# Kernel tuning notes

Hardware: AMD Instinct MI355X
Metric: run time of the kernel (lower is better)

## Reference

```python
import jax, jax.numpy as jnp
import numpy as np

BN_EPS = 1e-5

def binarize(v):
    # sign binarization with straight-through estimator (grad clipped to |v|<=1),
    # matching the Binarize autograd function used by BinarizeConv2d.
    c = jnp.clip(v, -1.0, 1.0)
    return c + jax.lax.stop_gradient(jnp.sign(v) - c)

def setup_inputs() -> dict:
    key = jax.random.key(0)
    kx, kw = jax.random.split(key)
    x = jax.random.normal(kx, (32, 64, 112, 112), dtype=jnp.float32)
    W = jax.random.normal(kw, (64, 64, 3, 3), dtype=jnp.float32) * 0.05
    gamma = jnp.ones((64,), dtype=jnp.float32)
    beta = jnp.zeros((64,), dtype=jnp.float32)
    return {"x": x, "W": W, "gamma": gamma, "beta": beta}

def reference(x, W, gamma, beta):
    residual = x
    # binet-style scaled binary conv: sign(x) * sign(W) conv, scaled per output
    # channel by alpha = mean(|W|) over (in, kh, kw)
    xb = binarize(x)
    wb = binarize(W)
    alpha = jnp.mean(jnp.abs(W), axis=(1, 2, 3))  # [Cout]
    out = jax.lax.conv_general_dilated(
        xb, wb,
        window_strides=(1, 1), padding=((1, 1), (1, 1)),
        dimension_numbers=("NCHW", "OIHW", "NCHW"))
    out = out * alpha[None, :, None, None]
    # BatchNorm2d (training mode: batch statistics over N,H,W)
    mu = jnp.mean(out, axis=(0, 2, 3), keepdims=True)
    var = jnp.var(out, axis=(0, 2, 3), keepdims=True)
    out = (out - mu) * jax.lax.rsqrt(var + BN_EPS)
    out = out * gamma[None, :, None, None] + beta[None, :, None, None]
    # Hardtanh
    out = jnp.clip(out, -1.0, 1.0)
    # residual add (downsample=None, stride=1)
    return out + residual
```

## Files before the change

### kernel.cpp

```cpp
#include <hip/hip_runtime.h>
#include <cstdint>

typedef unsigned long long u64;

#define HW    12544
#define NCH   64
#define NBATCH 32
#define NPIX  401408

__global__ __launch_bounds__(256) void k_pack(const float* __restrict__ x,
                                              const float* __restrict__ Wt,
                                              u64* __restrict__ xbits,
                                              u64* __restrict__ wbits,
                                              float* __restrict__ alpha) {
  int b = blockIdx.x;
  int t = threadIdx.x;
  if (b < 1568) {
    int n = b / 49;
    int p = (b % 49) * 256 + t;
    const float* xp = x + (size_t)n * NCH * HW + p;
    u64 m = 0;
#pragma unroll 16
    for (int c = 0; c < 64; ++c) {
      m |= (u64)(xp[(size_t)c * HW] > 0.0f) << c;
    }
    xbits[(size_t)n * HW + p] = m;
  } else {
    int wv = t >> 6, lane = t & 63;
    for (int i = 0; i < 16; ++i) {
      int co = wv * 16 + i;
      const float* wp = Wt + ((size_t)co * 64 + lane) * 9;
      float w9[9];
      float s = 0.0f;
#pragma unroll
      for (int k = 0; k < 9; ++k) { w9[k] = wp[k]; s += fabsf(w9[k]); }
#pragma unroll
      for (int off = 32; off > 0; off >>= 1) s += __shfl_xor(s, off);
#pragma unroll
      for (int k = 0; k < 9; ++k) {
        u64 msk = __ballot(w9[k] > 0.0f);
        if (lane == 0) wbits[k * 64 + co] = msk;
      }
      if (lane == 0) alpha[co] = s * (1.0f / 576.0f);
    }
  }
}

__global__ __launch_bounds__(256) void k_stats(const u64* __restrict__ xbits,
                                               const u64* __restrict__ wbits,
                                               u64* __restrict__ S1,
                                               u64* __restrict__ S2) {
  __shared__ u64 stg[4][114];
  __shared__ int corr[9][64];
  __shared__ int red1[256];
  __shared__ int red2[256];
  int b = blockIdx.x, t = threadIdx.x;
  int n = b / 56, h0 = (b % 56) * 2;

  for (int i = t; i < 4 * 114; i += 256) {
    int r = i / 114, cc = i % 114;
    int h = h0 - 1 + r, w = cc - 1;
    u64 v = 0;
    if (h >= 0 && h < 112 && (unsigned)w < 112u)
      v = xbits[(size_t)n * HW + h * 112 + w];
    stg[r][cc] = v;
  }

  int c = t & 63, wv = t >> 6;
  u64 wm[9];
#pragma unroll
  for (int k = 0; k < 9; ++k) wm[k] = wbits[k * 64 + c];

  if (t < 64) {
    int pw[9];
#pragma unroll
    for (int k = 0; k < 9; ++k) pw[k] = __popcll(wm[k]);
#pragma unroll
    for (int ht = 0; ht < 3; ++ht)
#pragma unroll
      for (int wt = 0; wt < 3; ++wt) {
        int s = 0;
#pragma unroll
        for (int k = 0; k < 9; ++k) {
          int dh = k / 3 - 1, dw = k % 3 - 1;
          bool inval = (ht == 0 && dh < 0) || (ht == 2 && dh > 0) ||
                       (wt == 0 && dw < 0) || (wt == 2 && dw > 0);
          if (inval) s += 64 - 2 * pw[k];
        }
        corr[ht * 3 + wt][t] = s;
      }
  }
  __syncthreads();

  int s1 = 0, s2 = 0;
  for (int k = 0; k < 56; ++k) {
    int pl = wv * 56 + k;
    int hl = pl / 112, w = pl % 112;
    int h = h0 + hl;
    int ht = (h == 0) ? 0 : ((h == 111) ? 2 : 1);
    int wt = (w == 0) ? 0 : ((w == 111) ? 2 : 1);
    int sum = 0;
#pragma unroll
    for (int kk = 0; kk < 9; ++kk)
      sum += __popcll(stg[hl + kk / 3][w + kk % 3] ^ wm[kk]);
    int I = 576 - 2 * sum - corr[ht * 3 + wt][c];
    s1 += I;
    s2 += I * I;
  }
  red1[t] = s1; red2[t] = s2;
  __syncthreads();
  if (t < 64) {
    int a1 = red1[t] + red1[t + 64] + red1[t + 128] + red1[t + 192];
    int a2 = red2[t] + red2[t + 64] + red2[t + 128] + red2[t + 192];
    atomicAdd(&S1[t], (u64)(long long)a1);
    atomicAdd(&S2[t], (u64)(long long)a2);
  }
}

__global__ __launch_bounds__(256) void k_final(const float* __restrict__ x,
                                               const u64* __restrict__ xbits,
                                               const u64* __restrict__ wbits,
                                               const u64* __restrict__ S1,
                                               const u64* __restrict__ S2,
                                               const float* __restrict__ alpha,
                                               const float* __restrict__ gamma,
                                               const float* __restrict__ beta,
                                               float* __restrict__ out) {
  __shared__ u64 stg[4][114];
  __shared__ u64 wsh[576];
  __shared__ int corr[9][64];
  __shared__ float scs[64];
  __shared__ float bis[64];
  int b = blockIdx.x, t = threadIdx.x;
  int n = b / 56, h0 = (b % 56) * 2;

  for (int i = t; i < 4 * 114; i += 256) {
    int r = i / 114, cc = i % 114;
    int h = h0 - 1 + r, w = cc - 1;
    u64 v = 0;
    if (h >= 0 && h < 112 && (unsigned)w < 112u)
      v = xbits[(size_t)n * HW + h * 112 + w];
    stg[r][cc] = v;
  }
  for (int i = t; i < 576; i += 256) wsh[i] = wbits[i];

  if (t < 64) {
    int pw[9];
#pragma unroll
    for (int k = 0; k < 9; ++k) pw[k] = __popcll(wbits[k * 64 + t]);
#pragma unroll
    for (int ht = 0; ht < 3; ++ht)
#pragma unroll
      for (int wt = 0; wt < 3; ++wt) {
        int s = 0;
#pragma unroll
        for (int k = 0; k < 9; ++k) {
          int dh = k / 3 - 1, dw = k % 3 - 1;
          bool inval = (ht == 0 && dh < 0) || (ht == 2 && dh > 0) ||
                       (wt == 0 && dw < 0) || (wt == 2 && dw > 0);
          if (inval) s += 64 - 2 * pw[k];
        }
        corr[ht * 3 + wt][t] = s;
      }
    long long s1 = (long long)S1[t];
    long long s2 = (long long)S2[t];
    double inv = 1.0 / (double)NPIX;
    double mean = (double)s1 * inv;
    double var = (double)s2 * inv - mean * mean;
    double al = (double)alpha[t];
    double rs = 1.0 / sqrt(al * al * var + 1e-5);
    double sc = (double)gamma[t] * al * rs;
    scs[t] = (float)sc;
    bis[t] = (float)((double)beta[t] - sc * mean);
  }
  __syncthreads();

  if (t < 224) {
    int hl = t / 112, w = t % 112;
    int h = h0 + hl;
    int ht = (h == 0) ? 0 : ((h == 111) ? 2 : 1);
    int wt = (w == 0) ? 0 : ((w == 111) ? 2 : 1);
    int type = ht * 3 + wt;
    u64 xm[9];
#pragma unroll
    for (int kk = 0; kk < 9; ++kk) xm[kk] = stg[hl + kk / 3][w + kk % 3];
    const float* xp = x + (size_t)n * NCH * HW + (size_t)h * 112 + w;
    float* op = out + (size_t)n * NCH * HW + (size_t)h * 112 + w;
#pragma unroll 4
    for (int c = 0; c < 64; ++c) {
      int sum = 0;
#pragma unroll
      for (int kk = 0; kk < 9; ++kk) sum += __popcll(xm[kk] ^ wsh[kk * 64 + c]);
      int I = 576 - 2 * sum - corr[type][c];
      float o = fmaf((float)I, scs[c], bis[c]);
      o = fminf(fmaxf(o, -1.0f), 1.0f);
      op[(size_t)c * HW] = o + xp[(size_t)c * HW];
    }
  }
}

extern "C" void kernel_launch(void* const* d_in, const int* in_sizes, int n_in,
                              void* d_out, int out_size, void* d_ws, size_t ws_size,
                              hipStream_t stream) {
  const float* x     = (const float*)d_in[0];
  const float* W     = (const float*)d_in[1];
  const float* gamma = (const float*)d_in[2];
  const float* beta  = (const float*)d_in[3];
  float* out = (float*)d_out;

  char* ws = (char*)d_ws;
  u64*  S1    = (u64*)(ws + 0);
  u64*  S2    = (u64*)(ws + 512);
  float* alpha = (float*)(ws + 1024);
  u64*  wbits = (u64*)(ws + 2048);
  u64*  xbits = (u64*)(ws + 8192);

  hipMemsetAsync(ws, 0, 1024, stream);

  hipLaunchKernelGGL(k_pack, dim3(1569), dim3(256), 0, stream, x, W, xbits, wbits, alpha);
  hipLaunchKernelGGL(k_stats, dim3(32 * 56), dim3(256), 0, stream, xbits, wbits, S1, S2);
  hipLaunchKernelGGL(k_final, dim3(32 * 56), dim3(256), 0, stream,
                     x, xbits, wbits, S1, S2, alpha, gamma, beta, out);
}
```

Baseline: 276.6 us.

## Register-block 4 rows per thread in binary conv kernels and vectorize packing

After: 266.8 us. 1.04x faster.

```diff
diff --git a/kernel.cpp b/kernel.cpp
--- a/kernel.cpp
+++ b/kernel.cpp
@@ -4,28 +4,34 @@
 typedef unsigned long long u64;
 
 #define HW    12544
-#define NCH   64
-#define NBATCH 32
 #define NPIX  401408
 
 __global__ __launch_bounds__(256) void k_pack(const float* __restrict__ x,
                                               const float* __restrict__ Wt,
                                               u64* __restrict__ xbits,
                                               u64* __restrict__ wbits,
-                                              float* __restrict__ alpha) {
+                                              float* __restrict__ alpha,
+                                              u64* __restrict__ stats) {
   int b = blockIdx.x;
   int t = threadIdx.x;
-  if (b < 1568) {
-    int n = b / 49;
-    int p = (b % 49) * 256 + t;
-    const float* xp = x + (size_t)n * NCH * HW + p;
-    u64 m = 0;
-#pragma unroll 16
+  if (b < 392) {
+    int gp = (b * 256 + t) * 4;
+    int n = gp / HW, p = gp % HW;
+    const float* xp = x + (size_t)n * 64 * HW + p;
+    u64 m0 = 0, m1 = 0, m2 = 0, m3 = 0;
+#pragma unroll 8
     for (int c = 0; c < 64; ++c) {
-      m |= (u64)(xp[(size_t)c * HW] > 0.0f) << c;
+      const float4 v = *reinterpret_cast<const float4*>(xp + (size_t)c * HW);
+      m0 |= (u64)(v.x > 0.0f) << c;
+      m1 |= (u64)(v.y > 0.0f) << c;
+      m2 |= (u64)(v.z > 0.0f) << c;
+      m3 |= (u64)(v.w > 0.0f) << c;
     }
-    xbits[(size_t)n * HW + p] = m;
+    ulonglong2* d2 = reinterpret_cast<ulonglong2*>(xbits + (size_t)n * HW + p);
+    d2[0] = make_ulonglong2(m0, m1);
+    d2[1] = make_ulonglong2(m2, m3);
   } else {
+    if (t < 128) stats[t] = 0;
     int wv = t >> 6, lane = t & 63;
     for (int i = 0; i < 16; ++i) {
       int co = wv * 16 + i;
@@ -50,70 +56,70 @@
                                                const u64* __restrict__ wbits,
                                                u64* __restrict__ S1,
                                                u64* __restrict__ S2) {
-  __shared__ u64 stg[4][114];
-  __shared__ int corr[9][64];
+  __shared__ u64 stg[10][114];
   __shared__ int red1[256];
   __shared__ int red2[256];
   int b = blockIdx.x, t = threadIdx.x;
-  int n = b / 56, h0 = (b % 56) * 2;
-
-  for (int i = t; i < 4 * 114; i += 256) {
+  int n = b / 14, h0 = (b % 14) * 8;
+
+  for (int i = t; i < 10 * 114; i += 256) {
     int r = i / 114, cc = i % 114;
     int h = h0 - 1 + r, w = cc - 1;
     u64 v = 0;
-    if (h >= 0 && h < 112 && (unsigned)w < 112u)
+    if ((unsigned)h < 112u && (unsigned)w < 112u)
       v = xbits[(size_t)n * HW + h * 112 + w];
     stg[r][cc] = v;
   }
 
   int c = t & 63, wv = t >> 6;
-  u64 wm[9];
-#pragma unroll
-  for (int k = 0; k < 9; ++k) wm[k] = wbits[k * 64 + c];
-
-  if (t < 64) {
-    int pw[9];
-#pragma unroll
-    for (int k = 0; k < 9; ++k) pw[k] = __popcll(wm[k]);
-#pragma unroll
-    for (int ht = 0; ht < 3; ++ht)
-#pragma unroll
-      for (int wt = 0; wt < 3; ++wt) {
-        int s = 0;
-#pragma unroll
-        for (int k = 0; k < 9; ++k) {
-          int dh = k / 3 - 1, dw = k % 3 - 1;
-          bool inval = (ht == 0 && dh < 0) || (ht == 2 && dh > 0) ||
-                       (wt == 0 && dw < 0) || (wt == 2 && dw > 0);
-          if (inval) s += 64 - 2 * pw[k];
-        }
-        corr[ht * 3 + wt][t] = s;
-      }
-  }
+  u64 wm0, wm1, wm2, wm3, wm4, wm5, wm6, wm7, wm8;
+  wm0 = wbits[0 * 64 + c]; wm1 = wbits[1 * 64 + c]; wm2 = wbits[2 * 64 + c];
+  wm3 = wbits[3 * 64 + c]; wm4 = wbits[4 * 64 + c]; wm5 = wbits[5 * 64 + c];
+  wm6 = wbits[6 * 64 + c]; wm7 = wbits[7 * 64 + c]; wm8 = wbits[8 * 64 + c];
+  int pw0 = __popcll(wm0), pw1 = __popcll(wm1), pw2 = __popcll(wm2);
+  int pw3 = __popcll(wm3), pw4 = __popcll(wm4), pw5 = __popcll(wm5);
+  int pw6 = __popcll(wm6), pw7 = __popcll(wm7), pw8 = __popcll(wm8);
+  int vtop = (64-2*pw0) + (64-2*pw1) + (64-2*pw2);
+  int vbot = (64-2*pw6) + (64-2*pw7) + (64-2*pw8);
+  int hlft = (64-2*pw0) + (64-2*pw3) + (64-2*pw6);
+  int hrgt = (64-2*pw2) + (64-2*pw5) + (64-2*pw8);
+  int cTL = 64-2*pw0, cTR = 64-2*pw2, cBL = 64-2*pw6, cBR = 64-2*pw8;
   __syncthreads();
 
   int s1 = 0, s2 = 0;
-  for (int k = 0; k < 56; ++k) {
-    int pl = wv * 56 + k;
-    int hl = pl / 112, w = pl % 112;
-    int h = h0 + hl;
-    int ht = (h == 0) ? 0 : ((h == 111) ? 2 : 1);
-    int wt = (w == 0) ? 0 : ((w == 111) ? 2 : 1);
-    int sum = 0;
-#pragma unroll
-    for (int kk = 0; kk < 9; ++kk)
-      sum += __popcll(stg[hl + kk / 3][w + kk % 3] ^ wm[kk]);
-    int I = 576 - 2 * sum - corr[ht * 3 + wt][c];
-    s1 += I;
-    s2 += I * I;
+  for (int it = 0; it < 56; ++it) {
+    int idx = wv * 56 + it;
+    int s = idx / 112, w = idx % 112;
+    int r0 = s * 4;
+    u64 a0 = stg[r0+0][w], a1 = stg[r0+0][w+1], a2 = stg[r0+0][w+2];
+    u64 b0 = stg[r0+1][w], b1 = stg[r0+1][w+1], b2 = stg[r0+1][w+2];
+    u64 c0 = stg[r0+2][w], c1 = stg[r0+2][w+1], c2 = stg[r0+2][w+2];
+    u64 d0 = stg[r0+3][w], d1 = stg[r0+3][w+1], d2 = stg[r0+3][w+2];
+    u64 e0 = stg[r0+4][w], e1 = stg[r0+4][w+1], e2 = stg[r0+4][w+2];
+    u64 f0 = stg[r0+5][w], f1 = stg[r0+5][w+1], f2 = stg[r0+5][w+2];
+    int wl = (w == 0), wr = (w == 111);
+    int hcor = wl ? hlft : (wr ? hrgt : 0);
+    int ctop = hcor, cbot = hcor;
+    if (h0 + s * 4 == 0)        ctop += vtop - (wl ? cTL : 0) - (wr ? cTR : 0);
+    if (h0 + s * 4 + 3 == 111)  cbot += vbot - (wl ? cBL : 0) - (wr ? cBR : 0);
+#define PX(x0,x1,x2,x3,x4,x5,x6,x7,x8,corr)                                    \
+    { int sum = __popcll((x0)^wm0)+__popcll((x1)^wm1)+__popcll((x2)^wm2)       \
+              + __popcll((x3)^wm3)+__popcll((x4)^wm4)+__popcll((x5)^wm5)       \
+              + __popcll((x6)^wm6)+__popcll((x7)^wm7)+__popcll((x8)^wm8);      \
+      int I = 576 - 2*sum - (corr); s1 += I; s2 += I*I; }
+    PX(a0,a1,a2,b0,b1,b2,c0,c1,c2, ctop);
+    PX(b0,b1,b2,c0,c1,c2,d0,d1,d2, hcor);
+    PX(c0,c1,c2,d0,d1,d2,e0,e1,e2, hcor);
+    PX(d0,d1,d2,e0,e1,e2,f0,f1,f2, cbot);
+#undef PX
   }
   red1[t] = s1; red2[t] = s2;
   __syncthreads();
   if (t < 64) {
-    int a1 = red1[t] + red1[t + 64] + red1[t + 128] + red1[t + 192];
-    int a2 = red2[t] + red2[t + 64] + red2[t + 128] + red2[t + 192];
-    atomicAdd(&S1[t], (u64)(long long)a1);
-    atomicAdd(&S2[t], (u64)(long long)a2);
+    int a1s = red1[t] + red1[t+64] + red1[t+128] + red1[t+192];
+    int a2s = red2[t] + red2[t+64] + red2[t+128] + red2[t+192];
+    atomicAdd(&S1[t], (u64)(long long)a1s);
+    atomicAdd(&S2[t], (u64)(long long)a2s);
   }
 }
 
@@ -126,19 +132,19 @@
                                                const float* __restrict__ gamma,
                                                const float* __restrict__ beta,
                                                float* __restrict__ out) {
-  __shared__ u64 stg[4][114];
+  __shared__ u64 stg[10][114];
   __shared__ u64 wsh[576];
-  __shared__ int corr[9][64];
+  __shared__ int corrs[9 * 64];
   __shared__ float scs[64];
   __shared__ float bis[64];
   int b = blockIdx.x, t = threadIdx.x;
-  int n = b / 56, h0 = (b % 56) * 2;
-
-  for (int i = t; i < 4 * 114; i += 256) {
+  int n = b / 14, h0 = (b % 14) * 8;
+
+  for (int i = t; i < 10 * 114; i += 256) {
     int r = i / 114, cc = i % 114;
     int h = h0 - 1 + r, w = cc - 1;
     u64 v = 0;
-    if (h >= 0 && h < 112 && (unsigned)w < 112u)
+    if ((unsigned)h < 112u && (unsigned)w < 112u)
       v = xbits[(size_t)n * HW + h * 112 + w];
     stg[r][cc] = v;
   }
@@ -160,7 +166,7 @@
                        (wt == 0 && dw < 0) || (wt == 2 && dw > 0);
           if (inval) s += 64 - 2 * pw[k];
         }
-        corr[ht * 3 + wt][t] = s;
+        corrs[(ht * 3 + wt) * 64 + t] = s;
       }
     long long s1 = (long long)S1[t];
     long long s2 = (long long)S2[t];
@@ -176,25 +182,50 @@
   __syncthreads();
 
   if (t < 224) {
-    int hl = t / 112, w = t % 112;
-    int h = h0 + hl;
-    int ht = (h == 0) ? 0 : ((h == 111) ? 2 : 1);
-    int wt = (w == 0) ? 0 : ((w == 111) ? 2 : 1);
-    int type = ht * 3 + wt;
-    u64 xm[9];
-#pragma unroll
-    for (int kk = 0; kk < 9; ++kk) xm[kk] = stg[hl + kk / 3][w + kk % 3];
-    const float* xp = x + (size_t)n * NCH * HW + (size_t)h * 112 + w;
-    float* op = out + (size_t)n * NCH * HW + (size_t)h * 112 + w;
-#pragma unroll 4
+    int w = t % 112, s = t / 112;
+    int r0 = s * 4;
+    int hb = h0 + s * 4;
+    u64 a0 = stg[r0+0][w], a1 = stg[r0+0][w+1], a2 = stg[r0+0][w+2];
+    u64 b0 = stg[r0+1][w], b1 = stg[r0+1][w+1], b2 = stg[r0+1][w+2];
+    u64 c0 = stg[r0+2][w], c1 = stg[r0+2][w+1], c2 = stg[r0+2][w+2];
+    u64 d0 = stg[r0+3][w], d1 = stg[r0+3][w+1], d2 = stg[r0+3][w+2];
+    u64 e0 = stg[r0+4][w], e1 = stg[r0+4][w+1], e2 = stg[r0+4][w+2];
+    u64 f0 = stg[r0+5][w], f1 = stg[r0+5][w+1], f2 = stg[r0+5][w+2];
+    int wl = (w == 0), wr = (w == 111);
+    int wt = wl ? 0 : (wr ? 2 : 1);
+    int ttop = ((hb == 0) ? 0 : 1) * 3 + wt;
+    int tmid = 3 + wt;
+    int tbot = ((hb + 3 == 111) ? 2 : 1) * 3 + wt;
+    const float* xp = x + (size_t)n * 64 * HW + (size_t)hb * 112 + w;
+    float* op = out + (size_t)n * 64 * HW + (size_t)hb * 112 + w;
+#pragma unroll 2
     for (int c = 0; c < 64; ++c) {
-      int sum = 0;
-#pragma unroll
-      for (int kk = 0; kk < 9; ++kk) sum += __popcll(xm[kk] ^ wsh[kk * 64 + c]);
-      int I = 576 - 2 * sum - corr[type][c];
-      float o = fmaf((float)I, scs[c], bis[c]);
-      o = fminf(fmaxf(o, -1.0f), 1.0f);
-      op[(size_t)c * HW] = o + xp[(size_t)c * HW];
+      int off = c * HW;
+      float x0 = xp[off], x1 = xp[off + 112], x2 = xp[off + 224], x3 = xp[off + 336];
+      u64 w0 = wsh[c],       w1 = wsh[64 + c],  w2 = wsh[128 + c];
+      u64 w3 = wsh[192 + c], w4 = wsh[256 + c], w5 = wsh[320 + c];
+      u64 w6 = wsh[384 + c], w7 = wsh[448 + c], w8 = wsh[512 + c];
+      float sc = scs[c], bi = bis[c];
+      int ct = corrs[ttop * 64 + c];
+      int cm = corrs[tmid * 64 + c];
+      int cb = corrs[tbot * 64 + c];
+#define SUM9(x0_,x1_,x2_,x3_,x4_,x5_,x6_,x7_,x8_)                              \
+      (__popcll((x0_)^w0)+__popcll((x1_)^w1)+__popcll((x2_)^w2)                \
+      +__popcll((x3_)^w3)+__popcll((x4_)^w4)+__popcll((x5_)^w5)                \
+      +__popcll((x6_)^w6)+__popcll((x7_)^w7)+__popcll((x8_)^w8))
+      int I0 = 576 - 2 * SUM9(a0,a1,a2,b0,b1,b2,c0,c1,c2) - ct;
+      int I1 = 576 - 2 * SUM9(b0,b1,b2,c0,c1,c2,d0,d1,d2) - cm;
+      int I2 = 576 - 2 * SUM9(c0,c1,c2,d0,d1,d2,e0,e1,e2) - cm;
+      int I3 = 576 - 2 * SUM9(d0,d1,d2,e0,e1,e2,f0,f1,f2) - cb;
+#undef SUM9
+      float o0 = fminf(fmaxf(fmaf((float)I0, sc, bi), -1.0f), 1.0f);
+      float o1 = fminf(fmaxf(fmaf((float)I1, sc, bi), -1.0f), 1.0f);
+      float o2 = fminf(fmaxf(fmaf((float)I2, sc, bi), -1.0f), 1.0f);
+      float o3 = fminf(fmaxf(fmaf((float)I3, sc, bi), -1.0f), 1.0f);
+      op[off]       = o0 + x0;
+      op[off + 112] = o1 + x1;
+      op[off + 224] = o2 + x2;
+      op[off + 336] = o3 + x3;
     }
   }
 }
@@ -209,16 +240,16 @@
   float* out = (float*)d_out;
 
   char* ws = (char*)d_ws;
-  u64*  S1    = (u64*)(ws + 0);
-  u64*  S2    = (u64*)(ws + 512);
+  u64*   S1    = (u64*)(ws + 0);
+  u64*   S2    = (u64*)(ws + 512);
   float* alpha = (float*)(ws + 1024);
-  u64*  wbits = (u64*)(ws + 2048);
-  u64*  xbits = (u64*)(ws + 8192);
-
-  hipMemsetAsync(ws, 0, 1024, stream);
-
-  hipLaunchKernelGGL(k_pack, dim3(1569), dim3(256), 0, stream, x, W, xbits, wbits, alpha);
-  hipLaunchKernelGGL(k_stats, dim3(32 * 56), dim3(256), 0, stream, xbits, wbits, S1, S2);
-  hipLaunchKernelGGL(k_final, dim3(32 * 56), dim3(256), 0, stream,
+  u64*   wbits = (u64*)(ws + 2048);
+  u64*   xbits = (u64*)(ws + 8192);
+
+  hipLaunchKernelGGL(k_pack, dim3(393), dim3(256), 0, stream,
+                     x, W, xbits, wbits, alpha, (u64*)ws);
+  hipLaunchKernelGGL(k_stats, dim3(32 * 14), dim3(256), 0, stream,
+                     xbits, wbits, S1, S2);
+  hipLaunchKernelGGL(k_final, dim3(32 * 14), dim3(256), 0, stream,
                      x, xbits, wbits, S1, S2, alpha, gamma, beta, out);
 }
```

## Replace popcount binary conv with int8 MFMA on zero-padded ±1 activations

Applied to the files above, without the earlier changes.

Measured after the change: 369.1 us. 33.4% more time.

```diff
diff --git a/kernel.cpp b/kernel.cpp
--- a/kernel.cpp
+++ b/kernel.cpp
@@ -2,200 +2,204 @@
 #include <cstdint>
 
 typedef unsigned long long u64;
-
-#define HW    12544
-#define NCH   64
-#define NBATCH 32
-#define NPIX  401408
+typedef unsigned int u32;
+typedef int v4i __attribute__((ext_vector_type(4)));
+
+#define HW   12544
+#define NPIX 401408
+#define PROW 114
+#define PRB  (PROW * 64)
+#define PNB  (114 * PRB)
 
 __global__ __launch_bounds__(256) void k_pack(const float* __restrict__ x,
-                                              const float* __restrict__ Wt,
-                                              u64* __restrict__ xbits,
-                                              u64* __restrict__ wbits,
-                                              float* __restrict__ alpha) {
-  int b = blockIdx.x;
-  int t = threadIdx.x;
-  if (b < 1568) {
-    int n = b / 49;
-    int p = (b % 49) * 256 + t;
-    const float* xp = x + (size_t)n * NCH * HW + p;
-    u64 m = 0;
-#pragma unroll 16
+                                              const float* __restrict__ W,
+                                              unsigned char* __restrict__ xi8,
+                                              unsigned char* __restrict__ wi8,
+                                              float* __restrict__ alpha9,
+                                              u64* __restrict__ stats) {
+  int b = blockIdx.x, t = threadIdx.x;
+  if (b < 392) {
+    int gp = (b * 256 + t) * 4;
+    int n = gp / HW, p = gp % HW;
+    int h = p / 112, w = p % 112;
+    const float* xp = x + (size_t)(n * 64) * HW + p;
+    u32 wd[4][16];
+#pragma unroll
+    for (int px = 0; px < 4; ++px)
+#pragma unroll
+      for (int q = 0; q < 16; ++q) wd[px][q] = 0;
+#pragma unroll
     for (int c = 0; c < 64; ++c) {
-      m |= (u64)(xp[(size_t)c * HW] > 0.0f) << c;
-    }
-    xbits[(size_t)n * HW + p] = m;
+      float4 v = *reinterpret_cast<const float4*>(xp + (size_t)c * HW);
+      u32 sh = (u32)(c & 3) * 8; int q = c >> 2;
+      wd[0][q] |= (v.x > 0.f ? 0x01u : 0xFFu) << sh;
+      wd[1][q] |= (v.y > 0.f ? 0x01u : 0xFFu) << sh;
+      wd[2][q] |= (v.z > 0.f ? 0x01u : 0xFFu) << sh;
+      wd[3][q] |= (v.w > 0.f ? 0x01u : 0xFFu) << sh;
+    }
+    uint4* sp = reinterpret_cast<uint4*>(
+        xi8 + (size_t)n * PNB + (size_t)(h + 1) * PRB + (size_t)(w + 1) * 64);
+#pragma unroll
+    for (int px = 0; px < 4; ++px)
+#pragma unroll
+      for (int q4 = 0; q4 < 4; ++q4)
+        sp[px * 4 + q4] = make_uint4(wd[px][4*q4], wd[px][4*q4+1],
+                                     wd[px][4*q4+2], wd[px][4*q4+3]);
   } else {
-    int wv = t >> 6, lane = t & 63;
-    for (int i = 0; i < 16; ++i) {
-      int co = wv * 16 + i;
-      const float* wp = Wt + ((size_t)co * 64 + lane) * 9;
-      float w9[9];
-      float s = 0.0f;
-#pragma unroll
-      for (int k = 0; k < 9; ++k) { w9[k] = wp[k]; s += fabsf(w9[k]); }
-#pragma unroll
-      for (int off = 32; off > 0; off >>= 1) s += __shfl_xor(s, off);
-#pragma unroll
-      for (int k = 0; k < 9; ++k) {
-        u64 msk = __ballot(w9[k] > 0.0f);
-        if (lane == 0) wbits[k * 64 + co] = msk;
+    if (t < 128) stats[t] = 0;
+    for (int i = t; i < 576; i += 256) {
+      int tap = i / 64, co = i % 64;
+      u32 wdw[16];
+#pragma unroll
+      for (int q = 0; q < 16; ++q) wdw[q] = 0;
+      float asum = 0.f;
+#pragma unroll
+      for (int ci = 0; ci < 64; ++ci) {
+        float wv = W[((size_t)co * 64 + ci) * 9 + tap];
+        asum += fabsf(wv);
+        wdw[ci >> 2] |= (wv > 0.f ? 0x01u : 0xFFu) << ((u32)(ci & 3) * 8);
       }
-      if (lane == 0) alpha[co] = s * (1.0f / 576.0f);
-    }
-  }
-}
-
-__global__ __launch_bounds__(256) void k_stats(const u64* __restrict__ xbits,
-                                               const u64* __restrict__ wbits,
-                                               u64* __restrict__ S1,
-                                               u64* __restrict__ S2) {
-  __shared__ u64 stg[4][114];
-  __shared__ int corr[9][64];
-  __shared__ int red1[256];
-  __shared__ int red2[256];
-  int b = blockIdx.x, t = threadIdx.x;
-  int n = b / 56, h0 = (b % 56) * 2;
-
-  for (int i = t; i < 4 * 114; i += 256) {
-    int r = i / 114, cc = i % 114;
-    int h = h0 - 1 + r, w = cc - 1;
-    u64 v = 0;
-    if (h >= 0 && h < 112 && (unsigned)w < 112u)
-      v = xbits[(size_t)n * HW + h * 112 + w];
-    stg[r][cc] = v;
-  }
-
-  int c = t & 63, wv = t >> 6;
-  u64 wm[9];
-#pragma unroll
-  for (int k = 0; k < 9; ++k) wm[k] = wbits[k * 64 + c];
-
-  if (t < 64) {
-    int pw[9];
-#pragma unroll
-    for (int k = 0; k < 9; ++k) pw[k] = __popcll(wm[k]);
-#pragma unroll
-    for (int ht = 0; ht < 3; ++ht)
-#pragma unroll
-      for (int wt = 0; wt < 3; ++wt) {
-        int s = 0;
-#pragma unroll
-        for (int k = 0; k < 9; ++k) {
-          int dh = k / 3 - 1, dw = k % 3 - 1;
-          bool inval = (ht == 0 && dh < 0) || (ht == 2 && dh > 0) ||
-                       (wt == 0 && dw < 0) || (wt == 2 && dw > 0);
-          if (inval) s += 64 - 2 * pw[k];
-        }
-        corr[ht * 3 + wt][t] = s;
-      }
-  }
-  __syncthreads();
-
-  int s1 = 0, s2 = 0;
-  for (int k = 0; k < 56; ++k) {
-    int pl = wv * 56 + k;
-    int hl = pl / 112, w = pl % 112;
-    int h = h0 + hl;
-    int ht = (h == 0) ? 0 : ((h == 111) ? 2 : 1);
-    int wt = (w == 0) ? 0 : ((w == 111) ? 2 : 1);
-    int sum = 0;
-#pragma unroll
-    for (int kk = 0; kk < 9; ++kk)
-      sum += __popcll(stg[hl + kk / 3][w + kk % 3] ^ wm[kk]);
-    int I = 576 - 2 * sum - corr[ht * 3 + wt][c];
-    s1 += I;
-    s2 += I * I;
-  }
-  red1[t] = s1; red2[t] = s2;
+      uint4* dp = reinterpret_cast<uint4*>(wi8 + tap * 4096 + co * 64);
+#pragma unroll
+      for (int q4 = 0; q4 < 4; ++q4)
+        dp[q4] = make_uint4(wdw[4*q4], wdw[4*q4+1], wdw[4*q4+2], wdw[4*q4+3]);
+      alpha9[i] = asum;
+    }
+  }
+}
+
+#define MFMA9(ACC0, ACC1, ACC2, ACC3)                                          \
+  _Pragma("unroll")                                                            \
+  for (int k = 0; k < 9; ++k) {                                                \
+    ACC0 = __builtin_amdgcn_mfma_i32_16x16x64_i8(A[0][k], B[k], ACC0, 0, 0, 0);\
+    ACC1 = __builtin_amdgcn_mfma_i32_16x16x64_i8(A[1][k], B[k], ACC1, 0, 0, 0);\
+    ACC2 = __builtin_amdgcn_mfma_i32_16x16x64_i8(A[2][k], B[k], ACC2, 0, 0, 0);\
+    ACC3 = __builtin_amdgcn_mfma_i32_16x16x64_i8(A[3][k], B[k], ACC3, 0, 0, 0);\
+  }
+
+__global__ __launch_bounds__(256, 2) void k_stats(const unsigned char* __restrict__ xi8,
+                                                  const unsigned char* __restrict__ wi8,
+                                                  u64* __restrict__ S1,
+                                                  u64* __restrict__ S2) {
+  __shared__ int sh1[4][64];
+  __shared__ int sh2[4][64];
+  int b = blockIdx.x, t = threadIdx.x, wv = t >> 6, l = t & 63;
+  int lo = (l & 15) * 64 + (l >> 4) * 16;
+  v4i A[4][9];
+#pragma unroll
+  for (int g = 0; g < 4; ++g)
+#pragma unroll
+    for (int k = 0; k < 9; ++k)
+      A[g][k] = *reinterpret_cast<const v4i*>(wi8 + k * 4096 + g * 1024 + lo);
+
+  int tid = b * 4 + wv;
+  int n = tid / 112, h = tid % 112;
+  const unsigned char* rowp = xi8 + (size_t)n * PNB + (size_t)(h + 1) * PRB + 64 + lo;
+  int s1a[4][4], s2a[4][4];
+#pragma unroll
+  for (int g = 0; g < 4; ++g)
+#pragma unroll
+    for (int j = 0; j < 4; ++j) { s1a[g][j] = 0; s2a[g][j] = 0; }
+
+  for (int wt = 0; wt < 7; ++wt) {
+    const unsigned char* bp = rowp + wt * 1024;
+    v4i B[9];
+#pragma unroll
+    for (int k = 0; k < 9; ++k) {
+      int dh = k / 3 - 1, dw = k % 3 - 1;
+      B[k] = *reinterpret_cast<const v4i*>(bp + dh * PRB + dw * 64);
+    }
+    v4i acc0 = {0,0,0,0}, acc1 = {0,0,0,0}, acc2 = {0,0,0,0}, acc3 = {0,0,0,0};
+    MFMA9(acc0, acc1, acc2, acc3)
+#define SEPI(G, ACC)                                                           \
+    _Pragma("unroll")                                                          \
+    for (int j = 0; j < 4; ++j) { int I = ACC[j]; s1a[G][j] += I; s2a[G][j] += I * I; }
+    SEPI(0, acc0) SEPI(1, acc1) SEPI(2, acc2) SEPI(3, acc3)
+#undef SEPI
+  }
+  int lo4 = (l >> 4) * 4;
+#pragma unroll
+  for (int g = 0; g < 4; ++g)
+#pragma unroll
+    for (int j = 0; j < 4; ++j) {
+      int v1 = s1a[g][j], v2 = s2a[g][j];
+      v1 += __shfl_xor(v1, 1); v1 += __shfl_xor(v1, 2);
+      v1 += __shfl_xor(v1, 4); v1 += __shfl_xor(v1, 8);
+      v2 += __shfl_xor(v2, 1); v2 += __shfl_xor(v2, 2);
+      v2 += __shfl_xor(v2, 4); v2 += __shfl_xor(v2, 8);
+      if ((l & 15) == 0) { int c = g * 16 + lo4 + j; sh1[wv][c] = v1; sh2[wv][c] = v2; }
+    }
   __syncthreads();
   if (t < 64) {
-    int a1 = red1[t] + red1[t + 64] + red1[t + 128] + red1[t + 192];
-    int a2 = red2[t] + red2[t + 64] + red2[t + 128] + red2[t + 192];
-    atomicAdd(&S1[t], (u64)(long long)a1);
-    atomicAdd(&S2[t], (u64)(long long)a2);
-  }
-}
-
-__global__ __launch_bounds__(256) void k_final(const float* __restrict__ x,
-                                               const u64* __restrict__ xbits,
-                                               const u64* __restrict__ wbits,
-                                               const u64* __restrict__ S1,
-                                               const u64* __restrict__ S2,
-                                               const float* __restrict__ alpha,
-                                               const float* __restrict__ gamma,
-                                               const float* __restrict__ beta,
-                                               float* __restrict__ out) {
-  __shared__ u64 stg[4][114];
-  __shared__ u64 wsh[576];
-  __shared__ int corr[9][64];
-  __shared__ float scs[64];
-  __shared__ float bis[64];
-  int b = blockIdx.x, t = threadIdx.x;
-  int n = b / 56, h0 = (b % 56) * 2;
-
-  for (int i = t; i < 4 * 114; i += 256) {
-    int r = i / 114, cc = i % 114;
-    int h = h0 - 1 + r, w = cc - 1;
-    u64 v = 0;
-    if (h >= 0 && h < 112 && (unsigned)w < 112u)
-      v = xbits[(size_t)n * HW + h * 112 + w];
-    stg[r][cc] = v;
-  }
-  for (int i = t; i < 576; i += 256) wsh[i] = wbits[i];
-
+    long long a1 = (long long)sh1[0][t] + sh1[1][t] + sh1[2][t] + sh1[3][t];
+    long long a2 = (long long)sh2[0][t] + sh2[1][t] + sh2[2][t] + sh2[3][t];
+    atomicAdd(&S1[t], (u64)a1);
+    atomicAdd(&S2[t], (u64)a2);
+  }
+}
+
+__global__ __launch_bounds__(256, 2) void k_final(const float* __restrict__ x,
+                                                  const unsigned char* __restrict__ xi8,
+                                                  const unsigned char* __restrict__ wi8,
+                                                  const u64* __restrict__ S1,
+                                                  const u64* __restrict__ S2,
+                                                  const float* __restrict__ alpha9,
+                                                  const float* __restrict__ gamma,
+                                                  const float* __restrict__ beta,
+                                                  float* __restrict__ out) {
+  __shared__ float2 scb[64];
+  int b = blockIdx.x, t = threadIdx.x, wv = t >> 6, l = t & 63;
   if (t < 64) {
-    int pw[9];
-#pragma unroll
-    for (int k = 0; k < 9; ++k) pw[k] = __popcll(wbits[k * 64 + t]);
-#pragma unroll
-    for (int ht = 0; ht < 3; ++ht)
-#pragma unroll
-      for (int wt = 0; wt < 3; ++wt) {
-        int s = 0;
-#pragma unroll
-        for (int k = 0; k < 9; ++k) {
-          int dh = k / 3 - 1, dw = k % 3 - 1;
-          bool inval = (ht == 0 && dh < 0) || (ht == 2 && dh > 0) ||
-                       (wt == 0 && dw < 0) || (wt == 2 && dw > 0);
-          if (inval) s += 64 - 2 * pw[k];
-        }
-        corr[ht * 3 + wt][t] = s;
-      }
-    long long s1 = (long long)S1[t];
-    long long s2 = (long long)S2[t];
+    float asum = 0.f;
+#pragma unroll
+    for (int k = 0; k < 9; ++k) asum += alpha9[k * 64 + t];
+    double al = (double)asum * (1.0 / 576.0);
+    long long s1v = (long long)S1[t], s2v = (long long)S2[t];
     double inv = 1.0 / (double)NPIX;
-    double mean = (double)s1 * inv;
-    double var = (double)s2 * inv - mean * mean;
-    double al = (double)alpha[t];
-    double rs = 1.0 / sqrt(al * al * var + 1e-5);
-    double sc = (double)gamma[t] * al * rs;
-    scs[t] = (float)sc;
-    bis[t] = (float)((double)beta[t] - sc * mean);
+    double mean = (double)s1v * inv;
+    double var = (double)s2v * inv - mean * mean;
+    double sc = (double)gamma[t] * al / sqrt(al * al * var + 1e-5);
+    scb[t] = make_float2((float)sc, (float)((double)beta[t] - sc * mean));
   }
   __syncthreads();
 
-  if (t < 224) {
-    int hl = t / 112, w = t % 112;
-    int h = h0 + hl;
-    int ht = (h == 0) ? 0 : ((h == 111) ? 2 : 1);
-    int wt = (w == 0) ? 0 : ((w == 111) ? 2 : 1);
-    int type = ht * 3 + wt;
-    u64 xm[9];
-#pragma unroll
-    for (int kk = 0; kk < 9; ++kk) xm[kk] = stg[hl + kk / 3][w + kk % 3];
-    const float* xp = x + (size_t)n * NCH * HW + (size_t)h * 112 + w;
-    float* op = out + (size_t)n * NCH * HW + (size_t)h * 112 + w;
-#pragma unroll 4
-    for (int c = 0; c < 64; ++c) {
-      int sum = 0;
-#pragma unroll
-      for (int kk = 0; kk < 9; ++kk) sum += __popcll(xm[kk] ^ wsh[kk * 64 + c]);
-      int I = 576 - 2 * sum - corr[type][c];
-      float o = fmaf((float)I, scs[c], bis[c]);
-      o = fminf(fmaxf(o, -1.0f), 1.0f);
-      op[(size_t)c * HW] = o + xp[(size_t)c * HW];
-    }
+  int lo = (l & 15) * 64 + (l >> 4) * 16;
+  v4i A[4][9];
+#pragma unroll
+  for (int g = 0; g < 4; ++g)
+#pragma unroll
+    for (int k = 0; k < 9; ++k)
+      A[g][k] = *reinterpret_cast<const v4i*>(wi8 + k * 4096 + g * 1024 + lo);
+
+  int tid = b * 4 + wv;
+  int n = tid / 112, h = tid % 112;
+  const unsigned char* rowp = xi8 + (size_t)n * PNB + (size_t)(h + 1) * PRB + 64 + lo;
+  size_t pixbase = (size_t)(n * 64) * HW + (size_t)h * 112 + (l & 15);
+  int lo4 = (l >> 4) * 4;
+
+  for (int wt = 0; wt < 7; ++wt) {
+    const unsigned char* bp = rowp + wt * 1024;
+    v4i B[9];
+#pragma unroll
+    for (int k = 0; k < 9; ++k) {
+      int dh = k / 3 - 1, dw = k % 3 - 1;
+      B[k] = *reinterpret_cast<const v4i*>(bp + dh * PRB + dw * 64);
+    }
+    v4i acc0 = {0,0,0,0}, acc1 = {0,0,0,0}, acc2 = {0,0,0,0}, acc3 = {0,0,0,0};
+    MFMA9(acc0, acc1, acc2, acc3)
+    size_t pb = pixbase + wt * 16;
+#define EPI(G, ACC)                                                            \
+    _Pragma("unroll")                                                          \
+    for (int j = 0; j < 4; ++j) {                                              \
+      int c = G * 16 + lo4 + j;                                                \
+      float2 sb = scb[c];                                                      \
+      float o = fmaf((float)ACC[j], sb.x, sb.y);                               \
+      o = fminf(fmaxf(o, -1.f), 1.f);                                          \
+      size_t a = pb + (size_t)c * HW;                                          \
+      out[a] = o + x[a];                                                       \
+    }
+    EPI(0, acc0) EPI(1, acc1) EPI(2, acc2) EPI(3, acc3)
+#undef EPI
   }
 }
 
@@ -209,16 +213,16 @@
   float* out = (float*)d_out;
 
   char* ws = (char*)d_ws;
-  u64*  S1    = (u64*)(ws + 0);
-  u64*  S2    = (u64*)(ws + 512);
-  float* alpha = (float*)(ws + 1024);
-  u64*  wbits = (u64*)(ws + 2048);
-  u64*  xbits = (u64*)(ws + 8192);
-
-  hipMemsetAsync(ws, 0, 1024, stream);
-
-  hipLaunchKernelGGL(k_pack, dim3(1569), dim3(256), 0, stream, x, W, xbits, wbits, alpha);
-  hipLaunchKernelGGL(k_stats, dim3(32 * 56), dim3(256), 0, stream, xbits, wbits, S1, S2);
-  hipLaunchKernelGGL(k_final, dim3(32 * 56), dim3(256), 0, stream,
-                     x, xbits, wbits, S1, S2, alpha, gamma, beta, out);
-}
+  u64*           S1     = (u64*)(ws + 0);
+  u64*           S2     = (u64*)(ws + 512);
+  float*         alpha9 = (float*)(ws + 1024);
+  unsigned char* wi8    = (unsigned char*)(ws + 4096);
+  unsigned char* xi8    = (unsigned char*)(ws + 65536);
+
+  hipMemsetAsync(xi8, 0, (size_t)32 * PNB, stream);
+  hipLaunchKernelGGL(k_pack, dim3(393), dim3(256), 0, stream,
+                     x, W, xi8, wi8, alpha9, (u64*)ws);
+  hipLaunchKernelGGL(k_stats, dim3(896), dim3(256), 0, stream, xi8, wi8, S1, S2);
+  hipLaunchKernelGGL(k_final, dim3(896), dim3(256), 0, stream,
+                     x, xi8, wi8, S1, S2, alpha9, gamma, beta, out);
+}
```
